# Optimization experiments

Measured on AMD Instinct MI355X. Metric: run time of the kernel, lower is better.

Reference implementation:

```python
import jax, jax.numpy as jnp
import numpy as np

B, N, D = 8, 1024, 768
H, HD = 12, 64


def setup_inputs() -> dict:
    key = jax.random.key(0)
    ks = jax.random.split(key, 9)
    return {
        "x": jax.random.normal(ks[0], (B, N, D), dtype=jnp.float32),
        "Wq": jax.random.normal(ks[1], (H, HD, HD), dtype=jnp.float32) * (HD ** -0.5),
        "Wk": jax.random.normal(ks[2], (H, HD, HD), dtype=jnp.float32) * (HD ** -0.5),
        "Wv": jax.random.normal(ks[3], (H, HD, HD), dtype=jnp.float32) * (HD ** -0.5),
        "bq": jax.random.normal(ks[4], (H, HD), dtype=jnp.float32) * 0.02,
        "bk": jax.random.normal(ks[5], (H, HD), dtype=jnp.float32) * 0.02,
        "bv": jax.random.normal(ks[6], (H, HD), dtype=jnp.float32) * 0.02,
        "Wo": jax.random.normal(ks[7], (D, D), dtype=jnp.float32) * (D ** -0.5),
        "bo": jnp.zeros((D,), dtype=jnp.float32),
    }


def reference(x, Wq, Wk, Wv, bq, bk, bv, Wo, bo):
    # x: [B, N, D]; split into H heads of size HD along the feature dim
    b, n, d = x.shape
    h, hd = Wq.shape[0], Wq.shape[1]
    xh = x.reshape(b, n, h, hd)
    # per-head linear projections (stacked nn.Linear(head_dim, head_dim))
    q = jnp.einsum('bnhd,hde->bhne', xh, Wq) + bq[None, :, None, :]
    k = jnp.einsum('bnhd,hde->bhne', xh, Wk) + bk[None, :, None, :]
    v = jnp.einsum('bnhd,hde->bhne', xh, Wv) + bv[None, :, None, :]
    # NOTE: faithful quirk - scale uses FULL dim, not head_dim
    scale = d ** -0.5
    scores = jnp.einsum('bhid,bhjd->bhij', q, k) * scale  # [B,H,N,N]
    attn = jax.nn.softmax(scores, axis=-1)
    out = jnp.einsum('bhij,bhjd->bhid', attn, v)  # [B,H,N,HD]
    out = out.transpose(0, 2, 1, 3).reshape(b, n, d)  # concat heads
    return out @ Wo.T + bo  # wO: nn.Linear(dim, dim)
```

## Files before the change

### kernel.cpp

```cpp
#include <hip/hip_runtime.h>


typedef __attribute__((ext_vector_type(8))) short short8;
typedef __attribute__((ext_vector_type(4))) float floatx4;

#define MFMA16(a, b, c) __builtin_amdgcn_mfma_f32_16x16x32_bf16((a), (b), (c), 0, 0, 0)

#if __has_builtin(__builtin_amdgcn_exp2f)
#define EXP2(x) __builtin_amdgcn_exp2f(x)
#else
#define EXP2(x) __expf(0.6931471805599453f * (x))
#endif
#if __has_builtin(__builtin_amdgcn_rcpf)
#define RCP(x) __builtin_amdgcn_rcpf(x)
#else
#define RCP(x) (1.0f / (x))
#endif

__device__ __forceinline__ unsigned short f2bf(float f) {
    union { float f; unsigned int i; } c;
    c.f = f;
    unsigned int i = c.i;
    return (unsigned short)((i + 0x7fffu + ((i >> 16) & 1u)) >> 16);
}
__device__ __forceinline__ unsigned short f2bf_trunc(float f) {
    union { float f; unsigned int i; } c;
    c.f = f;
    return (unsigned short)(c.i >> 16);
}

__global__ __launch_bounds__(256) void prep_weights(
    const float* __restrict__ Wq, const float* __restrict__ Wk,
    const float* __restrict__ Wv, const float* __restrict__ Wo,
    unsigned short* __restrict__ Wqt, unsigned short* __restrict__ Wkt,
    unsigned short* __restrict__ Wvt, unsigned short* __restrict__ Wob)
{
    int tid = blockIdx.x * 256 + threadIdx.x;
    if (tid < 49152) {
        int h = tid >> 12, r = tid & 4095;
        int e = r >> 6, k = r & 63;
        int src = h * 4096 + k * 64 + e, dst = h * 4096 + e * 64 + k;
        Wqt[dst] = f2bf(Wq[src]);
        Wkt[dst] = f2bf(Wk[src]);
        Wvt[dst] = f2bf(Wv[src]);
    }
    for (int i = tid; i < 589824; i += 147456) Wob[i] = f2bf(Wo[i]);
}

__global__ __launch_bounds__(256) void qkv_proj(
    const float* __restrict__ x,
    const unsigned short* __restrict__ Wqt, const unsigned short* __restrict__ Wkt,
    const unsigned short* __restrict__ Wvt,
    const float* __restrict__ bq, const float* __restrict__ bk,
    const float* __restrict__ bv,
    unsigned short* __restrict__ Q, unsigned short* __restrict__ K,
    unsigned short* __restrict__ Vt)
{
    __shared__ __align__(16) unsigned short xlds[64 * 72];
    __shared__ __align__(16) unsigned short vlds[64 * 72];

    const int bh = blockIdx.y;
    const int b = bh / 12, h = bh % 12;
    const int wave = threadIdx.x >> 6, lane = threadIdx.x & 63;
    const int lrow = lane & 15, quad = lane >> 4;
    const int row0 = blockIdx.x * 64;
    const float scale = 0.052058776672f;

    {
        const int tr = threadIdx.x >> 4;
        const int tc = (threadIdx.x & 15) * 4;
        #pragma unroll
        for (int rr = 0; rr < 4; ++rr) {
            const int r = tr + rr * 16;
            const float* src = x + ((size_t)(b * 1024 + row0 + r)) * 768
                               + h * 64 + tc;
            float4 f = *(const float4*)src;
            unsigned short pkd[4];
            pkd[0] = f2bf(f.x); pkd[1] = f2bf(f.y);
            pkd[2] = f2bf(f.z); pkd[3] = f2bf(f.w);
            *(uint2*)&xlds[r * 72 + tc] = *(uint2*)pkd;
        }
    }
    __syncthreads();

    short8 xb0 = *(const short8*)&xlds[(wave * 16 + lrow) * 72 + quad * 8];
    short8 xb1 = *(const short8*)&xlds[(wave * 16 + lrow) * 72 + 32 + quad * 8];

    const floatx4 zero = { 0.f, 0.f, 0.f, 0.f };

    const unsigned short* Wm[2] = { Wqt + h * 4096, Wkt + h * 4096 };
    const float* bm[2] = { bq + h * 64, bk + h * 64 };
    unsigned short* Om[2] = {
        Q + ((size_t)bh * 1024 + row0 + wave * 16 + lrow) * 64,
        K + ((size_t)bh * 1024 + row0 + wave * 16 + lrow) * 64 };
    #pragma unroll
    for (int m = 0; m < 2; ++m) {
        const unsigned short* W = Wm[m];
        #pragma unroll
        for (int t = 0; t < 4; ++t) {
            short8 wa0 = *(const short8*)(W + (t * 16 + lrow) * 64 + quad * 8);
            short8 wa1 = *(const short8*)(W + (t * 16 + lrow) * 64 + 32 + quad * 8);
            floatx4 acc = zero;
            acc = MFMA16(wa0, xb0, acc);
            acc = MFMA16(wa1, xb1, acc);
            float4 bias = *(const float4*)(bm[m] + t * 16 + quad * 4);
            const float bs[4] = { bias.x, bias.y, bias.z, bias.w };
            unsigned short pkd[4];
            #pragma unroll
            for (int r = 0; r < 4; ++r) {
                float v = acc[r] + bs[r];
                if (m == 0) v *= scale;
                pkd[r] = f2bf(v);
            }
            *(uint2*)(Om[m] + t * 16 + quad * 4) = *(uint2*)pkd;
        }
    }

    {
        const unsigned short* W = Wvt + h * 4096;
        const float* bvh = bv + h * 64;
        #pragma unroll
        for (int t = 0; t < 4; ++t) {
            short8 wa0 = *(const short8*)(W + (t * 16 + lrow) * 64 + quad * 8);
            short8 wa1 = *(const short8*)(W + (t * 16 + lrow) * 64 + 32 + quad * 8);
            floatx4 acc = zero;
            acc = MFMA16(wa0, xb0, acc);
            acc = MFMA16(wa1, xb1, acc);
            float4 bias = *(const float4*)(bvh + t * 16 + quad * 4);
            const float bs[4] = { bias.x, bias.y, bias.z, bias.w };
            #pragma unroll
            for (int r = 0; r < 4; ++r)
                vlds[(t * 16 + quad * 4 + r) * 72 + wave * 16 + lrow]
                    = f2bf(acc[r] + bs[r]);
        }
    }
    __syncthreads();
    {
        const int er = threadIdx.x >> 2;
        const int sc = threadIdx.x & 3;
        short8 v0 = *(const short8*)&vlds[er * 72 + sc * 16];
        short8 v1 = *(const short8*)&vlds[er * 72 + sc * 16 + 8];
        unsigned short* dst = Vt + (size_t)bh * 65536 + (size_t)er * 1024
                              + row0 + sc * 16;
        *(short8*)dst = v0;
        *(short8*)(dst + 8) = v1;
    }
}

__global__ __launch_bounds__(256) void attn_kernel(
    const unsigned short* __restrict__ Q, const unsigned short* __restrict__ K,
    const unsigned short* __restrict__ Vt, unsigned short* __restrict__ AO)
{
    __shared__ __align__(16) unsigned short Klds[64 * 72];
    __shared__ __align__(16) unsigned short Vlds[64 * 72];

    const int bh = (int)blockIdx.x + ((int)blockIdx.y >> 3) * 8;
    const int qb = blockIdx.y & 7;
    const int b = bh / 12, h = bh % 12;
    const int wave = threadIdx.x >> 6, lane = threadIdx.x & 63;
    const int lrow = lane & 15, quad = lane >> 4;
    const int qrow0 = qb * 128 + wave * 32;

    const unsigned short* Qb = Q + (size_t)bh * 65536;
    const unsigned short* Kb = K + (size_t)bh * 65536;
    const unsigned short* Vb = Vt + (size_t)bh * 65536;

    const int tch = threadIdx.x & 7, trow = threadIdx.x >> 3;
    const int slot0 = ((trow & 4) << 2) | ((trow >> 3) << 2) | (trow & 3);

    short8 aq[2][2];
    #pragma unroll
    for (int mm = 0; mm < 2; ++mm) {
        const unsigned short* qr = Qb + (size_t)(qrow0 + mm * 16 + lrow) * 64;
        aq[mm][0] = *(const short8*)(qr + quad * 8);
        aq[mm][1] = *(const short8*)(qr + 32 + quad * 8);
    }

    const floatx4 zero = { 0.f, 0.f, 0.f, 0.f };
    float part[2] = { 0.f, 0.f };
    floatx4 Oacc[2][4];
    #pragma unroll
    for (int mm = 0; mm < 2; ++mm)
        #pragma unroll
        for (int t = 0; t < 4; ++t) Oacc[mm][t] = zero;

    short8 kpre[2], vpre[2];
    kpre[0] = *(const short8*)(Kb + (size_t)trow * 64 + tch * 8);
    kpre[1] = *(const short8*)(Kb + (size_t)(trow + 32) * 64 + tch * 8);
    vpre[0] = *(const short8*)(Vb + (size_t)trow * 1024 + tch * 8);
    vpre[1] = *(const short8*)(Vb + (size_t)(trow + 32) * 1024 + tch * 8);

    for (int jt = 0; jt < 16; ++jt) {
        *(short8*)&Klds[slot0 * 72 + tch * 8] = kpre[0];
        *(short8*)&Klds[(slot0 + 32) * 72 + tch * 8] = kpre[1];
        *(short8*)&Vlds[trow * 72 + tch * 8] = vpre[0];
        *(short8*)&Vlds[(trow + 32) * 72 + tch * 8] = vpre[1];
        __syncthreads();

        {
            const int jn = ((jt + 1) & 15) * 64;
            kpre[0] = *(const short8*)(Kb + (size_t)(jn + trow) * 64 + tch * 8);
            kpre[1] = *(const short8*)(Kb + (size_t)(jn + trow + 32) * 64 + tch * 8);
            vpre[0] = *(const short8*)(Vb + (size_t)trow * 1024 + jn + tch * 8);
            vpre[1] = *(const short8*)(Vb + (size_t)(trow + 32) * 1024 + jn + tch * 8);
        }

        #pragma unroll
        for (int w = 0; w < 2; ++w) {
            short8 kA[2][2];
            #pragma unroll
            for (int tau = 0; tau < 2; ++tau) {
                int kr = w * 32 + tau * 16 + lrow;
                kA[tau][0] = *(const short8*)&Klds[kr * 72 + quad * 8];
                kA[tau][1] = *(const short8*)&Klds[kr * 72 + 32 + quad * 8];
            }
            short8 vA[4];
            #pragma unroll
            for (int t = 0; t < 4; ++t)
                vA[t] = *(const short8*)&Vlds[(t * 16 + lrow) * 72
                                              + w * 32 + quad * 8];

            #pragma unroll
            for (int mm = 0; mm < 2; ++mm) {
                floatx4 s0 = zero, s1 = zero;
                s0 = MFMA16(kA[0][0], aq[mm][0], s0);
                s0 = MFMA16(kA[0][1], aq[mm][1], s0);
                s1 = MFMA16(kA[1][0], aq[mm][0], s1);
                s1 = MFMA16(kA[1][1], aq[mm][1], s1);

                short8 pk;
                #pragma unroll
                for (int r = 0; r < 4; ++r) {
                    float p0 = EXP2(s0[r]);
                    float p1 = EXP2(s1[r]);
                    part[mm] += p0 + p1;
                    pk[r] = (short)f2bf_trunc(p0);
                    pk[4 + r] = (short)f2bf_trunc(p1);
                }
                #pragma unroll
                for (int t = 0; t < 4; ++t)
                    Oacc[mm][t] = MFMA16(vA[t], pk, Oacc[mm][t]);
            }
        }
        __syncthreads();
    }

    #pragma unroll
    for (int mm = 0; mm < 2; ++mm) {
        float ts = part[mm];
        ts += __shfl_xor(ts, 16);
        ts += __shfl_xor(ts, 32);
        float inv = RCP(ts);
        unsigned short* orow = AO
            + ((size_t)(b * 1024 + qrow0 + mm * 16 + lrow)) * 768 + h * 64;
        #pragma unroll
        for (int t = 0; t < 4; ++t) {
            unsigned short pkd[4];
            #pragma unroll
            for (int r = 0; r < 4; ++r)
                pkd[r] = f2bf(Oacc[mm][t][r] * inv);
            *(uint2*)(orow + t * 16 + quad * 4) = *(uint2*)pkd;
        }
    }
}

__global__ __launch_bounds__(256) void out_proj(
    const unsigned short* __restrict__ AO, const unsigned short* __restrict__ Wob,
    const float* __restrict__ bo, float* __restrict__ Y)
{
    __shared__ __align__(16) unsigned short Alds[128 * 72];
    __shared__ __align__(16) unsigned short Blds[64 * 72];

    const int wave = threadIdx.x >> 6, lane = threadIdx.x & 63;
    const int lrow = lane & 15, quad = lane >> 4;
    const int row0 = blockIdx.x * 128;
    const int c0 = blockIdx.y * 64;
    const int wrow = (wave >> 1) * 64, wcol = (wave & 1) * 32;

    const int tch = threadIdx.x & 7, trow = threadIdx.x >> 3;

    const floatx4 zero = { 0.f, 0.f, 0.f, 0.f };
    floatx4 acc[2][4];
    #pragma unroll
    for (int u = 0; u < 2; ++u)
        #pragma unroll
        for (int t = 0; t < 4; ++t) acc[u][t] = zero;

    short8 apre[4], bpre[2];
    #pragma unroll
    for (int rr = 0; rr < 4; ++rr)
        apre[rr] = *(const short8*)(AO + (size_t)(row0 + trow + rr * 32) * 768
                                    + tch * 8);
    #pragma unroll
    for (int rr = 0; rr < 2; ++rr)
        bpre[rr] = *(const short8*)(Wob + (size_t)(c0 + trow + rr * 32) * 768
                                    + tch * 8);

    for (int k0 = 0; k0 < 768; k0 += 64) {
        #pragma unroll
        for (int rr = 0; rr < 4; ++rr)
            *(short8*)&Alds[(trow + rr * 32) * 72 + tch * 8] = apre[rr];
        #pragma unroll
        for (int rr = 0; rr < 2; ++rr)
            *(short8*)&Blds[(trow + rr * 32) * 72 + tch * 8] = bpre[rr];
        __syncthreads();

        {
            const int kn = (k0 + 64 < 768) ? k0 + 64 : 0;
            #pragma unroll
            for (int rr = 0; rr < 4; ++rr)
                apre[rr] = *(const short8*)(AO
                    + (size_t)(row0 + trow + rr * 32) * 768 + kn + tch * 8);
            #pragma unroll
            for (int rr = 0; rr < 2; ++rr)
                bpre[rr] = *(const short8*)(Wob
                    + (size_t)(c0 + trow + rr * 32) * 768 + kn + tch * 8);
        }

        #pragma unroll
        for (int kc = 0; kc < 2; ++kc) {
            short8 aoF[4], wF[2];
            #pragma unroll
            for (int t = 0; t < 4; ++t)
                aoF[t] = *(const short8*)&Alds[(wrow + t * 16 + lrow) * 72
                                               + kc * 32 + quad * 8];
            #pragma unroll
            for (int u = 0; u < 2; ++u)
                wF[u] = *(const short8*)&Blds[(wcol + u * 16 + lrow) * 72
                                              + kc * 32 + quad * 8];
            #pragma unroll
            for (int u = 0; u < 2; ++u)
                #pragma unroll
                for (int t = 0; t < 4; ++t)
                    acc[u][t] = MFMA16(wF[u], aoF[t], acc[u][t]);
        }
        __syncthreads();
    }

    #pragma unroll
    for (int u = 0; u < 2; ++u) {
        const int cb = c0 + wcol + u * 16 + quad * 4;
        float4 bias = *(const float4*)(bo + cb);
        const float bs[4] = { bias.x, bias.y, bias.z, bias.w };
        #pragma unroll
        for (int t = 0; t < 4; ++t) {
            const int row = row0 + wrow + t * 16 + lrow;
            float out[4];
            #pragma unroll
            for (int r = 0; r < 4; ++r) out[r] = acc[u][t][r] + bs[r];
            *(float4*)(Y + (size_t)row * 768 + cb) = *(float4*)out;
        }
    }
}

extern "C" void kernel_launch(void* const* d_in, const int* in_sizes, int n_in,
                              void* d_out, int out_size, void* d_ws, size_t ws_size,
                              hipStream_t stream)
{
    const float* x  = (const float*)d_in[0];
    const float* Wq = (const float*)d_in[1];
    const float* Wk = (const float*)d_in[2];
    const float* Wv = (const float*)d_in[3];
    const float* bq = (const float*)d_in[4];
    const float* bk = (const float*)d_in[5];
    const float* bv = (const float*)d_in[6];
    const float* Wo = (const float*)d_in[7];
    const float* bo = (const float*)d_in[8];

    unsigned short* Q   = (unsigned short*)d_ws;
    unsigned short* K   = Q + 6291456;
    unsigned short* Vt  = K + 6291456;
    unsigned short* AO  = Vt + 6291456;
    unsigned short* Wqt = AO + 6291456;
    unsigned short* Wkt = Wqt + 49152;
    unsigned short* Wvt = Wkt + 49152;
    unsigned short* Wob = Wvt + 49152;
    float* Y = (float*)d_out;

    prep_weights<<<dim3(576), 256, 0, stream>>>(Wq, Wk, Wv, Wo, Wqt, Wkt, Wvt, Wob);
    qkv_proj<<<dim3(16, 96), 256, 0, stream>>>(x, Wqt, Wkt, Wvt, bq, bk, bv, Q, K, Vt);
    attn_kernel<<<dim3(8, 96), 256, 0, stream>>>(Q, K, Vt, AO);
    out_proj<<<dim3(64, 12), 256, 0, stream>>>(AO, Wob, bo, Y);
}
```

Baseline: 169.6 us.

## Double-buffer attention LDS, compute row sums via MFMA, fuse Wo conversion into out_proj

The attention kernel now double-buffers its K/V shared-memory tiles, so the next tile is written after compute and only one barrier is needed per iteration. The softmax denominator now comes from an extra MFMA against a ones vector instead of scalar adds and cross-lane shuffles, which sums the truncated bf16 probabilities. The separate bf16 conversion pass over Wo is removed: out_proj reads fp32 Wo directly and converts each tile in registers, trading smaller prep work for double the weight bytes loaded per out_proj block and more conversion ALU work.

```diff
diff --git a/kernel.cpp b/kernel.cpp
--- a/kernel.cpp
+++ b/kernel.cpp
@@ -31,20 +31,17 @@
 
 __global__ __launch_bounds__(256) void prep_weights(
     const float* __restrict__ Wq, const float* __restrict__ Wk,
-    const float* __restrict__ Wv, const float* __restrict__ Wo,
+    const float* __restrict__ Wv,
     unsigned short* __restrict__ Wqt, unsigned short* __restrict__ Wkt,
-    unsigned short* __restrict__ Wvt, unsigned short* __restrict__ Wob)
+    unsigned short* __restrict__ Wvt)
 {
     int tid = blockIdx.x * 256 + threadIdx.x;
-    if (tid < 49152) {
-        int h = tid >> 12, r = tid & 4095;
-        int e = r >> 6, k = r & 63;
-        int src = h * 4096 + k * 64 + e, dst = h * 4096 + e * 64 + k;
-        Wqt[dst] = f2bf(Wq[src]);
-        Wkt[dst] = f2bf(Wk[src]);
-        Wvt[dst] = f2bf(Wv[src]);
-    }
-    for (int i = tid; i < 589824; i += 147456) Wob[i] = f2bf(Wo[i]);
+    int h = tid >> 12, r = tid & 4095;
+    int e = r >> 6, k = r & 63;
+    int src = h * 4096 + k * 64 + e, dst = h * 4096 + e * 64 + k;
+    Wqt[dst] = f2bf(Wq[src]);
+    Wkt[dst] = f2bf(Wk[src]);
+    Wvt[dst] = f2bf(Wv[src]);
 }
 
 __global__ __launch_bounds__(256) void qkv_proj(
@@ -151,8 +148,8 @@
     const unsigned short* __restrict__ Q, const unsigned short* __restrict__ K,
     const unsigned short* __restrict__ Vt, unsigned short* __restrict__ AO)
 {
-    __shared__ __align__(16) unsigned short Klds[64 * 72];
-    __shared__ __align__(16) unsigned short Vlds[64 * 72];
+    __shared__ __align__(16) unsigned short Klds[2][64 * 72];
+    __shared__ __align__(16) unsigned short Vlds[2][64 * 72];
 
     const int bh = (int)blockIdx.x + ((int)blockIdx.y >> 3) * 8;
     const int qb = blockIdx.y & 7;
@@ -177,7 +174,9 @@
     }
 
     const floatx4 zero = { 0.f, 0.f, 0.f, 0.f };
-    float part[2] = { 0.f, 0.f };
+    const short S1 = (short)0x3F80;
+    const short8 ones = { S1, S1, S1, S1, S1, S1, S1, S1 };
+    floatx4 acc_s[2] = { zero, zero };
     floatx4 Oacc[2][4];
     #pragma unroll
     for (int mm = 0; mm < 2; ++mm)
@@ -189,13 +188,14 @@
     kpre[1] = *(const short8*)(Kb + (size_t)(trow + 32) * 64 + tch * 8);
     vpre[0] = *(const short8*)(Vb + (size_t)trow * 1024 + tch * 8);
     vpre[1] = *(const short8*)(Vb + (size_t)(trow + 32) * 1024 + tch * 8);
+    *(short8*)&Klds[0][slot0 * 72 + tch * 8] = kpre[0];
+    *(short8*)&Klds[0][(slot0 + 32) * 72 + tch * 8] = kpre[1];
+    *(short8*)&Vlds[0][trow * 72 + tch * 8] = vpre[0];
+    *(short8*)&Vlds[0][(trow + 32) * 72 + tch * 8] = vpre[1];
+    __syncthreads();
 
     for (int jt = 0; jt < 16; ++jt) {
-        *(short8*)&Klds[slot0 * 72 + tch * 8] = kpre[0];
-        *(short8*)&Klds[(slot0 + 32) * 72 + tch * 8] = kpre[1];
-        *(short8*)&Vlds[trow * 72 + tch * 8] = vpre[0];
-        *(short8*)&Vlds[(trow + 32) * 72 + tch * 8] = vpre[1];
-        __syncthreads();
+        const int buf = jt & 1;
 
         {
             const int jn = ((jt + 1) & 15) * 64;
@@ -211,14 +211,14 @@
             #pragma unroll
             for (int tau = 0; tau < 2; ++tau) {
                 int kr = w * 32 + tau * 16 + lrow;
-                kA[tau][0] = *(const short8*)&Klds[kr * 72 + quad * 8];
-                kA[tau][1] = *(const short8*)&Klds[kr * 72 + 32 + quad * 8];
+                kA[tau][0] = *(const short8*)&Klds[buf][kr * 72 + quad * 8];
+                kA[tau][1] = *(const short8*)&Klds[buf][kr * 72 + 32 + quad * 8];
             }
             short8 vA[4];
             #pragma unroll
             for (int t = 0; t < 4; ++t)
-                vA[t] = *(const short8*)&Vlds[(t * 16 + lrow) * 72
-                                              + w * 32 + quad * 8];
+                vA[t] = *(const short8*)&Vlds[buf][(t * 16 + lrow) * 72
+                                                   + w * 32 + quad * 8];
 
             #pragma unroll
             for (int mm = 0; mm < 2; ++mm) {
@@ -231,26 +231,26 @@
                 short8 pk;
                 #pragma unroll
                 for (int r = 0; r < 4; ++r) {
-                    float p0 = EXP2(s0[r]);
-                    float p1 = EXP2(s1[r]);
-                    part[mm] += p0 + p1;
-                    pk[r] = (short)f2bf_trunc(p0);
-                    pk[4 + r] = (short)f2bf_trunc(p1);
+                    pk[r] = (short)f2bf_trunc(EXP2(s0[r]));
+                    pk[4 + r] = (short)f2bf_trunc(EXP2(s1[r]));
                 }
                 #pragma unroll
                 for (int t = 0; t < 4; ++t)
                     Oacc[mm][t] = MFMA16(vA[t], pk, Oacc[mm][t]);
+                acc_s[mm] = MFMA16(ones, pk, acc_s[mm]);
             }
         }
+
+        *(short8*)&Klds[buf ^ 1][slot0 * 72 + tch * 8] = kpre[0];
+        *(short8*)&Klds[buf ^ 1][(slot0 + 32) * 72 + tch * 8] = kpre[1];
+        *(short8*)&Vlds[buf ^ 1][trow * 72 + tch * 8] = vpre[0];
+        *(short8*)&Vlds[buf ^ 1][(trow + 32) * 72 + tch * 8] = vpre[1];
         __syncthreads();
     }
 
     #pragma unroll
     for (int mm = 0; mm < 2; ++mm) {
-        float ts = part[mm];
-        ts += __shfl_xor(ts, 16);
-        ts += __shfl_xor(ts, 32);
-        float inv = RCP(ts);
+        float inv = RCP(acc_s[mm][0]);
         unsigned short* orow = AO
             + ((size_t)(b * 1024 + qrow0 + mm * 16 + lrow)) * 768 + h * 64;
         #pragma unroll
@@ -265,7 +265,7 @@
 }
 
 __global__ __launch_bounds__(256) void out_proj(
-    const unsigned short* __restrict__ AO, const unsigned short* __restrict__ Wob,
+    const unsigned short* __restrict__ AO, const float* __restrict__ Wo,
     const float* __restrict__ bo, float* __restrict__ Y)
 {
     __shared__ __align__(16) unsigned short Alds[128 * 72];
@@ -286,23 +286,32 @@
         #pragma unroll
         for (int t = 0; t < 4; ++t) acc[u][t] = zero;
 
-    short8 apre[4], bpre[2];
+    short8 apre[4];
+    float4 bpre[2][2];
     #pragma unroll
     for (int rr = 0; rr < 4; ++rr)
         apre[rr] = *(const short8*)(AO + (size_t)(row0 + trow + rr * 32) * 768
                                     + tch * 8);
     #pragma unroll
-    for (int rr = 0; rr < 2; ++rr)
-        bpre[rr] = *(const short8*)(Wob + (size_t)(c0 + trow + rr * 32) * 768
-                                    + tch * 8);
+    for (int rr = 0; rr < 2; ++rr) {
+        const float* src = Wo + (size_t)(c0 + trow + rr * 32) * 768 + tch * 8;
+        bpre[rr][0] = *(const float4*)src;
+        bpre[rr][1] = *(const float4*)(src + 4);
+    }
 
     for (int k0 = 0; k0 < 768; k0 += 64) {
         #pragma unroll
         for (int rr = 0; rr < 4; ++rr)
             *(short8*)&Alds[(trow + rr * 32) * 72 + tch * 8] = apre[rr];
         #pragma unroll
-        for (int rr = 0; rr < 2; ++rr)
-            *(short8*)&Blds[(trow + rr * 32) * 72 + tch * 8] = bpre[rr];
+        for (int rr = 0; rr < 2; ++rr) {
+            unsigned short pkd[8];
+            pkd[0] = f2bf(bpre[rr][0].x); pkd[1] = f2bf(bpre[rr][0].y);
+            pkd[2] = f2bf(bpre[rr][0].z); pkd[3] = f2bf(bpre[rr][0].w);
+            pkd[4] = f2bf(bpre[rr][1].x); pkd[5] = f2bf(bpre[rr][1].y);
+            pkd[6] = f2bf(bpre[rr][1].z); pkd[7] = f2bf(bpre[rr][1].w);
+            *(short8*)&Blds[(trow + rr * 32) * 72 + tch * 8] = *(short8*)pkd;
+        }
         __syncthreads();
 
         {
@@ -312,9 +321,12 @@
                 apre[rr] = *(const short8*)(AO
                     + (size_t)(row0 + trow + rr * 32) * 768 + kn + tch * 8);
             #pragma unroll
-            for (int rr = 0; rr < 2; ++rr)
-                bpre[rr] = *(const short8*)(Wob
-                    + (size_t)(c0 + trow + rr * 32) * 768 + kn + tch * 8);
+            for (int rr = 0; rr < 2; ++rr) {
+                const float* src = Wo + (size_t)(c0 + trow + rr * 32) * 768
+                                   + kn + tch * 8;
+                bpre[rr][0] = *(const float4*)src;
+                bpre[rr][1] = *(const float4*)(src + 4);
+            }
         }
 
         #pragma unroll
@@ -374,11 +386,11 @@
     unsigned short* Wqt = AO + 6291456;
     unsigned short* Wkt = Wqt + 49152;
     unsigned short* Wvt = Wkt + 49152;
-    unsigned short* Wob = Wvt + 49152;
+
     float* Y = (float*)d_out;
 
-    prep_weights<<<dim3(576), 256, 0, stream>>>(Wq, Wk, Wv, Wo, Wqt, Wkt, Wvt, Wob);
+    prep_weights<<<dim3(192), 256, 0, stream>>>(Wq, Wk, Wv, Wqt, Wkt, Wvt);
     qkv_proj<<<dim3(16, 96), 256, 0, stream>>>(x, Wqt, Wkt, Wvt, bq, bk, bv, Q, K, Vt);
     attn_kernel<<<dim3(8, 96), 256, 0, stream>>>(Q, K, Vt, AO);
-    out_proj<<<dim3(64, 12), 256, 0, stream>>>(AO, Wob, bo, Y);
-}
+    out_proj<<<dim3(64, 12), 256, 0, stream>>>(AO, Wo, bo, Y);
+}
```

Result: slower. 173.2 us (+2.1%).
